# Kernel optimization log

Measured on AMD Instinct MI355X. Metric: run time of the kernel, lower is better.

## Reference

```python
import jax, jax.numpy as jnp
import numpy as np

N_NODES = 100000


def gcn_conv(x, W, b, src, dst, n):
    # PyG GCNConv: linear transform, add self-loops, symmetric degree normalization,
    # scatter-add aggregation from src -> dst, then bias.
    h = x @ W  # [N, F_out]
    loop = jnp.arange(n, dtype=src.dtype)
    s = jnp.concatenate([src, loop])  # sources incl. self-loops
    d = jnp.concatenate([dst, loop])  # targets incl. self-loops
    deg = jax.ops.segment_sum(jnp.ones_like(d, dtype=h.dtype), d, num_segments=n)
    dinv = jnp.where(deg > 0, jax.lax.rsqrt(deg), 0.0)
    norm = dinv[s] * dinv[d]  # [E+N]
    msg = h[s] * norm[:, None]  # gather + scale
    out = jax.ops.segment_sum(msg, d, num_segments=n)  # scatter-add
    return out + b


def setup_inputs() -> dict:
    key = jax.random.key(0)
    k1, k2, k3, k4 = jax.random.split(key, 4)
    n, e = N_NODES, 1600000
    z = jax.random.normal(k1, (n, 64), dtype=jnp.float32)
    edge_index = jax.random.randint(k2, (2, e), 0, n, dtype=jnp.int64)
    # Glorot-ish init for weights, zero bias (PyG default bias init is zeros)
    W1 = jax.random.normal(k3, (64, 128), dtype=jnp.float32) * (1.0 / np.sqrt(64))
    b1 = jnp.zeros((128,), dtype=jnp.float32)
    W2 = jax.random.normal(k4, (128, 64), dtype=jnp.float32) * (1.0 / np.sqrt(128))
    b2 = jnp.zeros((64,), dtype=jnp.float32)
    return {"z": z, "edge_index": edge_index, "W1": W1, "b1": b1, "W2": W2, "b2": b2}


def reference(z, edge_index, W1, b1, W2, b2):
    n = z.shape[0]
    src, dst = edge_index[0], edge_index[1]
    h = gcn_conv(z, W1, b1, src, dst, n)
    h = jax.nn.relu(h)
    x_hat = gcn_conv(h, W2, b2, src, dst, n)
    return x_hat
```

## Files before the change

### kernel.cpp

```cpp
#include <hip/hip_runtime.h>
#include <hip/hip_bf16.h>


#define WAVE 64
#define BSHIFT 8
#define NPB 256
#define CAP 5120
#define CH 4096
#define NBMAX 512

typedef __attribute__((ext_vector_type(8))) short bf16x8;
typedef __attribute__((ext_vector_type(4))) float f32x4;

__device__ inline float bf16_to_f32(unsigned short h) {
    return __uint_as_float(((unsigned int)h) << 16);
}
__device__ inline unsigned short f32_to_bf16(float f) {
    unsigned int x = __float_as_uint(f);
    return (unsigned short)((x + 0x7FFFu + ((x >> 16) & 1u)) >> 16);
}

__device__ inline float gather_rows16(const unsigned short* __restrict__ hs,
                                      const int* __restrict__ csr,
                                      int beg, int end, int lane, int zrow,
                                      float acc)
{
    for (int e = beg; e < end; e += 16) {
        int s[16];
#pragma unroll
        for (int j = 0; j < 16; ++j) s[j] = csr[e + j];
#pragma unroll
        for (int j = 0; j < 16; ++j)
            s[j] = (e + j < end) ? s[j] : zrow;
        float v[16];
#pragma unroll
        for (int j = 0; j < 16; ++j)
            v[j] = bf16_to_f32(hs[(size_t)s[j] * 64 + lane]);
        float t0 = ((v[0] + v[1]) + (v[2] + v[3])) + ((v[4] + v[5]) + (v[6] + v[7]));
        float t1 = ((v[8] + v[9]) + (v[10] + v[11])) + ((v[12] + v[13]) + (v[14] + v[15]));
        acc += t0 + t1;
    }
    return acc;
}

__global__ void prep(const float* __restrict__ W1, const float* __restrict__ W2,
                     unsigned short* __restrict__ W1t, unsigned short* __restrict__ W2t,
                     int* __restrict__ bcursor, int NB,
                     unsigned short* __restrict__ zr, int N)
{
    int i = blockIdx.x * blockDim.x + threadIdx.x;
    if (i < NB) bcursor[i] = 0;
    if (i < 64) zr[(size_t)N * 64 + i] = 0;
    if (i < 128 * 64) {
        int n = i >> 6, k = i & 63;
        W1t[i] = f32_to_bf16(W1[k * 128 + n]);
    }
    if (i < 64 * 128) {
        int n = i >> 7, k = i & 127;
        W2t[i] = f32_to_bf16(W2[k * 64 + n]);
    }
}

__global__ __launch_bounds__(256) void bin_edges(
        const int* __restrict__ src, const int* __restrict__ dst,
        int* __restrict__ bcursor, int2* __restrict__ ebuf, int E, int NB)
{
    __shared__ int hist[NBMAX];
    __shared__ int cur[NBMAX];
    const int t  = threadIdx.x;
    const int e0 = blockIdx.x * CH;

    for (int b = t; b < NB; b += 256) hist[b] = 0;
    __syncthreads();

#pragma unroll
    for (int j = 0; j < CH / 256; ++j) {
        int e = e0 + j * 256 + t;
        if (e < E) atomicAdd(&hist[dst[e] >> BSHIFT], 1);
    }
    __syncthreads();

    for (int b = t; b < NB; b += 256) {
        int c = hist[b];
        cur[b] = (c > 0) ? atomicAdd(&bcursor[b], c) : 0;
    }
    __syncthreads();

#pragma unroll
    for (int j = 0; j < CH / 256; ++j) {
        int e = e0 + j * 256 + t;
        if (e < E) {
            int s = src[e], d = dst[e];
            int b = d >> BSHIFT;
            int pos = atomicAdd(&cur[b], 1);
            ebuf[(size_t)b * CAP + pos] = make_int2(s, d);
        }
    }
}

__global__ __launch_bounds__(256) void build_csr(
        const int2* __restrict__ ebuf, const int* __restrict__ bcursor,
        const float* __restrict__ z, float* __restrict__ dinv,
        int* __restrict__ rbeg, int* __restrict__ rend,
        int* __restrict__ csr, unsigned short* __restrict__ u, int N)
{
    __shared__ int   h[NPB];
    __shared__ int   tmp[NPB];
    __shared__ float sdv[NPB];
    const int t   = threadIdx.x;
    const int b   = blockIdx.x;
    const int n0  = b << BSHIFT;
    const int cnt = bcursor[b];
    const size_t base = (size_t)b * CAP;

    h[t] = 0;
    __syncthreads();

    for (int i = t; i < cnt; i += 256)
        atomicAdd(&h[ebuf[base + i].y - n0], 1);
    __syncthreads();

    int deg = h[t];
    tmp[t] = deg;
    __syncthreads();
    for (int off = 1; off < 256; off <<= 1) {
        int x = (t >= off) ? tmp[t - off] : 0;
        __syncthreads();
        tmp[t] += x;
        __syncthreads();
    }
    int st = tmp[t] - deg;

    int node = n0 + t;
    float di = rsqrtf((float)deg + 1.0f);
    sdv[t] = di;
    if (node < N) {
        dinv[node] = di;
        rbeg[node] = (int)base + st;
        rend[node] = (int)base + st + deg;
    }
    h[t] = st;
    __syncthreads();

    for (int i = t; i < cnt; i += 256) {
        int2 e = ebuf[base + i];
        int p = atomicAdd(&h[e.y - n0], 1);
        csr[base + p] = e.x;
    }

    const int nloc = (N - n0 < NPB) ? (N - n0) : NPB;
    for (int i = t; i < nloc * 16; i += 256) {
        int r = i >> 4, kq = i & 15;
        float d2 = sdv[r];
        float4 v = ((const float4*)(z + (size_t)(n0 + r) * 64))[kq];
        ushort4 o;
        o.x = f32_to_bf16(v.x * d2);
        o.y = f32_to_bf16(v.y * d2);
        o.z = f32_to_bf16(v.z * d2);
        o.w = f32_to_bf16(v.w * d2);
        ((ushort4*)(u + (size_t)(n0 + r) * 64))[kq] = o;
    }
}

template<bool POST>
__global__ __launch_bounds__(256) void aggregate64_bf16(
        const unsigned short* __restrict__ hs, const int* __restrict__ rbeg,
        const int* __restrict__ rend, const int* __restrict__ csr,
        const float* __restrict__ dinv, const float* __restrict__ b,
        void* __restrict__ out_, int N)
{
    int node = (int)((blockIdx.x * (size_t)blockDim.x + threadIdx.x) >> 6);
    int lane = threadIdx.x & 63;
    if (node >= N) return;
    node = __builtin_amdgcn_readfirstlane(node);

    const int beg = rbeg[node];
    const int end = rend[node];

    float acc = bf16_to_f32(hs[(size_t)node * 64 + lane]);
    acc = gather_rows16(hs, csr, beg, end, lane, N, acc);

    if (POST) {
        float o = dinv[node] * acc + b[lane];
        __builtin_nontemporal_store(o, &((float*)out_)[(size_t)node * 64 + lane]);
    } else {
        __builtin_nontemporal_store(f32_to_bf16(acc),
            &((unsigned short*)out_)[(size_t)node * 64 + lane]);
    }
}

#define TILE 32
#define W1T_ST 72
#define W2T_ST 136
#define A_ST   72
#define X1_ST  136

__global__ __launch_bounds__(256) void gemm12_mfma(
        const unsigned short* __restrict__ agg1,
        const unsigned short* __restrict__ W1t,
        const float* __restrict__ b1,
        const unsigned short* __restrict__ W2t,
        const float* __restrict__ dinv,
        unsigned short* __restrict__ hs2, int N)
{
    __shared__ unsigned short sW1[128 * W1T_ST];
    __shared__ unsigned short sW2[64 * W2T_ST];
    __shared__ unsigned short sA[TILE * A_ST];
    __shared__ unsigned short sX[TILE * X1_ST];
    __shared__ float sdv[TILE];

    const int tid  = threadIdx.x;
    const int row0 = blockIdx.x * TILE;
    const int lane = tid & 63;
    const int wv   = tid >> 6;
    const int l16  = lane & 15;
    const int quad = lane >> 4;

    for (int i = tid; i < 128 * 8; i += 256) {
        int r = i >> 3, c = i & 7;
        *(uint4*)&sW1[r * W1T_ST + c * 8] = *(const uint4*)&W1t[r * 64 + c * 8];
    }
    for (int i = tid; i < 64 * 16; i += 256) {
        int r = i >> 4, c = i & 15;
        *(uint4*)&sW2[r * W2T_ST + c * 8] = *(const uint4*)&W2t[r * 128 + c * 8];
    }
    for (int i = tid; i < TILE * 8; i += 256) {
        int r = i >> 3, c = i & 7;
        int gr = row0 + r;
        uint4 v = make_uint4(0u, 0u, 0u, 0u);
        if (gr < N) v = *(const uint4*)&agg1[(size_t)gr * 64 + c * 8];
        *(uint4*)&sA[r * A_ST + c * 8] = v;
    }
    if (tid < TILE) {
        int gr = row0 + tid;
        sdv[tid] = (gr < N) ? dinv[gr] : 0.0f;
    }
    __syncthreads();

    {
        const int mt  = wv & 1;
        const int ntb = (wv >> 1) * 4;
        f32x4 acc[4];
#pragma unroll
        for (int t = 0; t < 4; ++t) acc[t] = (f32x4)0.0f;

#pragma unroll
        for (int k0 = 0; k0 < 64; k0 += 32) {
            bf16x8 af = *(const bf16x8*)&sA[(mt * 16 + l16) * A_ST + k0 + quad * 8];
#pragma unroll
            for (int t = 0; t < 4; ++t) {
                bf16x8 bf = *(const bf16x8*)&sW1[((ntb + t) * 16 + l16) * W1T_ST + k0 + quad * 8];
                acc[t] = __builtin_amdgcn_mfma_f32_16x16x32_bf16(af, bf, acc[t], 0, 0, 0);
            }
        }

#pragma unroll
        for (int t = 0; t < 4; ++t) {
            int col = (ntb + t) * 16 + l16;
            float bb = b1[col];
#pragma unroll
            for (int r = 0; r < 4; ++r) {
                int lr = mt * 16 + quad * 4 + r;
                float o = fmaxf(acc[t][r] * sdv[lr] + bb, 0.0f);
                sX[lr * X1_ST + col] = f32_to_bf16(o);
            }
        }
    }
    __syncthreads();

    {
        const int mt  = wv & 1;
        const int ntb = (wv >> 1) * 2;
        f32x4 acc[2];
#pragma unroll
        for (int t = 0; t < 2; ++t) acc[t] = (f32x4)0.0f;

#pragma unroll
        for (int k0 = 0; k0 < 128; k0 += 32) {
            bf16x8 af = *(const bf16x8*)&sX[(mt * 16 + l16) * X1_ST + k0 + quad * 8];
#pragma unroll
            for (int t = 0; t < 2; ++t) {
                bf16x8 bf = *(const bf16x8*)&sW2[((ntb + t) * 16 + l16) * W2T_ST + k0 + quad * 8];
                acc[t] = __builtin_amdgcn_mfma_f32_16x16x32_bf16(af, bf, acc[t], 0, 0, 0);
            }
        }

#pragma unroll
        for (int t = 0; t < 2; ++t) {
            int col = (ntb + t) * 16 + l16;
#pragma unroll
            for (int r = 0; r < 4; ++r) {
                int lr = mt * 16 + quad * 4 + r;
                int gr = row0 + lr;
                if (gr < N)
                    hs2[(size_t)gr * 64 + col] = f32_to_bf16(acc[t][r] * sdv[lr]);
            }
        }
    }
}

static inline size_t align_up(size_t x, size_t a) { return (x + a - 1) / a * a; }

extern "C" void kernel_launch(void* const* d_in, const int* in_sizes, int n_in,
                              void* d_out, int out_size, void* d_ws, size_t ws_size,
                              hipStream_t stream) {
    const float* z    = (const float*)d_in[0];
    const int*   eidx = (const int*)d_in[1];
    const float* W1   = (const float*)d_in[2];
    const float* b1   = (const float*)d_in[3];
    const float* W2   = (const float*)d_in[4];
    const float* b2   = (const float*)d_in[5];
    float* out = (float*)d_out;

    const int N = in_sizes[0] / 64;
    const int E = in_sizes[1] / 2;
    const int* src = eidx;
    const int* dst = eidx + E;
    const int NB = (N + NPB - 1) >> BSHIFT;

    char* ws = (char*)d_ws;
    size_t off = 0;
    float* dinv    = (float*)(ws + off); off = align_up(off + (size_t)N * 4, 512);
    int*   rbeg    = (int*)  (ws + off); off = align_up(off + (size_t)N * 4, 512);
    int*   rend    = (int*)  (ws + off); off = align_up(off + (size_t)N * 4, 512);
    int*   bcursor = (int*)  (ws + off); off = align_up(off + (size_t)NBMAX * 4, 512);
    unsigned short* W1t = (unsigned short*)(ws + off); off = align_up(off + 8192 * 2, 512);
    unsigned short* W2t = (unsigned short*)(ws + off); off = align_up(off + 8192 * 2, 512);
    int*   csr     = (int*)  (ws + off); off = align_up(off + (size_t)NB * CAP * 4, 512);
    float* bufA    = (float*)(ws + off); off = align_up(off + (size_t)N * 64 * 4, 512);
    float* bufB    = (float*)(ws + off); off = align_up(off + (size_t)N * 64 * 4, 512);
    float* bufC    = (float*)(ws + off); off = align_up(off + (size_t)N * 128 * 4, 512);
    (void)ws_size;

    unsigned short* u    = (unsigned short*)bufA;
    unsigned short* agg1 = (unsigned short*)bufB;
    unsigned short* hs2  = (unsigned short*)bufA;
    int2*  ebuf    = (int2*)bufC;

    prep<<<32, 256, 0, stream>>>(W1, W2, W1t, W2t, bcursor, NB, u, N);

    bin_edges<<<(E + CH - 1) / CH, 256, 0, stream>>>(src, dst, bcursor, ebuf, E, NB);
    build_csr<<<NB, 256, 0, stream>>>(ebuf, bcursor, z, dinv, rbeg, rend, csr, u, N);

    aggregate64_bf16<false><<<(N + 3) / 4, 256, 0, stream>>>(u, rbeg, rend, csr, dinv, nullptr, agg1, N);

    gemm12_mfma<<<(N + TILE - 1) / TILE, 256, 0, stream>>>(agg1, W1t, b1, W2t, dinv, hs2, N);

    aggregate64_bf16<true><<<(N + 3) / 4, 256, 0, stream>>>(hs2, rbeg, rend, csr, dinv, b2, out, N);
}
```

Measured before the change: 236.9 us.

## Pack binned edges into 32-bit words and aggregate two nodes per wavefront

Edge binning now stores each edge as one 32-bit word: the source index sits in the low 24 bits and the destination's offset within its bin in the high 8 bits. This halves the ebuf write and read traffic between bin_edges and build_csr. The aggregation kernels now process two nodes per wavefront with interleaved gathers, putting more independent loads in flight. The packing assumes node ids fit in 24 bits, and the paired loop runs to the longer row, so it pads the shorter one with zero-row gathers.

```diff
diff --git a/kernel.cpp b/kernel.cpp
--- a/kernel.cpp
+++ b/kernel.cpp
@@ -20,29 +20,6 @@
     return (unsigned short)((x + 0x7FFFu + ((x >> 16) & 1u)) >> 16);
 }
 
-__device__ inline float gather_rows16(const unsigned short* __restrict__ hs,
-                                      const int* __restrict__ csr,
-                                      int beg, int end, int lane, int zrow,
-                                      float acc)
-{
-    for (int e = beg; e < end; e += 16) {
-        int s[16];
-#pragma unroll
-        for (int j = 0; j < 16; ++j) s[j] = csr[e + j];
-#pragma unroll
-        for (int j = 0; j < 16; ++j)
-            s[j] = (e + j < end) ? s[j] : zrow;
-        float v[16];
-#pragma unroll
-        for (int j = 0; j < 16; ++j)
-            v[j] = bf16_to_f32(hs[(size_t)s[j] * 64 + lane]);
-        float t0 = ((v[0] + v[1]) + (v[2] + v[3])) + ((v[4] + v[5]) + (v[6] + v[7]));
-        float t1 = ((v[8] + v[9]) + (v[10] + v[11])) + ((v[12] + v[13]) + (v[14] + v[15]));
-        acc += t0 + t1;
-    }
-    return acc;
-}
-
 __global__ void prep(const float* __restrict__ W1, const float* __restrict__ W2,
                      unsigned short* __restrict__ W1t, unsigned short* __restrict__ W2t,
                      int* __restrict__ bcursor, int NB,
@@ -63,7 +40,7 @@
 
 __global__ __launch_bounds__(256) void bin_edges(
         const int* __restrict__ src, const int* __restrict__ dst,
-        int* __restrict__ bcursor, int2* __restrict__ ebuf, int E, int NB)
+        int* __restrict__ bcursor, unsigned int* __restrict__ ebuf, int E, int NB)
 {
     __shared__ int hist[NBMAX];
     __shared__ int cur[NBMAX];
@@ -93,13 +70,14 @@
             int s = src[e], d = dst[e];
             int b = d >> BSHIFT;
             int pos = atomicAdd(&cur[b], 1);
-            ebuf[(size_t)b * CAP + pos] = make_int2(s, d);
+            ebuf[(size_t)b * CAP + pos] =
+                (unsigned int)s | ((unsigned int)(d & (NPB - 1)) << 24);
         }
     }
 }
 
 __global__ __launch_bounds__(256) void build_csr(
-        const int2* __restrict__ ebuf, const int* __restrict__ bcursor,
+        const unsigned int* __restrict__ ebuf, const int* __restrict__ bcursor,
         const float* __restrict__ z, float* __restrict__ dinv,
         int* __restrict__ rbeg, int* __restrict__ rend,
         int* __restrict__ csr, unsigned short* __restrict__ u, int N)
@@ -117,7 +95,7 @@
     __syncthreads();
 
     for (int i = t; i < cnt; i += 256)
-        atomicAdd(&h[ebuf[base + i].y - n0], 1);
+        atomicAdd(&h[ebuf[base + i] >> 24], 1);
     __syncthreads();
 
     int deg = h[t];
@@ -143,9 +121,9 @@
     __syncthreads();
 
     for (int i = t; i < cnt; i += 256) {
-        int2 e = ebuf[base + i];
-        int p = atomicAdd(&h[e.y - n0], 1);
-        csr[base + p] = e.x;
+        unsigned int w = ebuf[base + i];
+        int p = atomicAdd(&h[w >> 24], 1);
+        csr[base + p] = (int)(w & 0xFFFFFFu);
     }
 
     const int nloc = (N - n0 < NPB) ? (N - n0) : NPB;
@@ -169,23 +147,65 @@
         const float* __restrict__ dinv, const float* __restrict__ b,
         void* __restrict__ out_, int N)
 {
-    int node = (int)((blockIdx.x * (size_t)blockDim.x + threadIdx.x) >> 6);
-    int lane = threadIdx.x & 63;
-    if (node >= N) return;
-    node = __builtin_amdgcn_readfirstlane(node);
-
-    const int beg = rbeg[node];
-    const int end = rend[node];
-
-    float acc = bf16_to_f32(hs[(size_t)node * 64 + lane]);
-    acc = gather_rows16(hs, csr, beg, end, lane, N, acc);
+    int pair = (int)((blockIdx.x * (size_t)blockDim.x + threadIdx.x) >> 6);
+    const int lane = threadIdx.x & 63;
+    int nA = pair * 2;
+    if (nA >= N) return;
+    nA = __builtin_amdgcn_readfirstlane(nA);
+    const int nBr = nA + 1;
+    const bool hasB = (nBr < N);
+    const int nB = hasB ? nBr : N;
+
+    const int begA = rbeg[nA], endA = rend[nA];
+    int begB = 0, endB = 0;
+    if (hasB) { begB = rbeg[nBr]; endB = rend[nBr]; }
+
+    float accA = bf16_to_f32(hs[(size_t)nA * 64 + lane]);
+    float accB = bf16_to_f32(hs[(size_t)nB * 64 + lane]);
+
+    int nbat = (endA - begA + 15) >> 4;
+    int nbB  = (endB - begB + 15) >> 4;
+    if (nbB > nbat) nbat = nbB;
+
+    int eA = begA, eB = begB;
+    for (int bt = 0; bt < nbat; ++bt, eA += 16, eB += 16) {
+        int sA[16], sB[16];
+#pragma unroll
+        for (int j = 0; j < 16; ++j) sA[j] = csr[eA + j];
+#pragma unroll
+        for (int j = 0; j < 16; ++j) sB[j] = csr[eB + j];
+#pragma unroll
+        for (int j = 0; j < 16; ++j) sA[j] = (eA + j < endA) ? sA[j] : N;
+#pragma unroll
+        for (int j = 0; j < 16; ++j) sB[j] = (eB + j < endB) ? sB[j] : N;
+        float vA[16], vB[16];
+#pragma unroll
+        for (int j = 0; j < 16; ++j)
+            vA[j] = bf16_to_f32(hs[(size_t)sA[j] * 64 + lane]);
+#pragma unroll
+        for (int j = 0; j < 16; ++j)
+            vB[j] = bf16_to_f32(hs[(size_t)sB[j] * 64 + lane]);
+        float a0 = ((vA[0]+vA[1])+(vA[2]+vA[3])) + ((vA[4]+vA[5])+(vA[6]+vA[7]));
+        float a1 = ((vA[8]+vA[9])+(vA[10]+vA[11])) + ((vA[12]+vA[13])+(vA[14]+vA[15]));
+        accA += a0 + a1;
+        float c0 = ((vB[0]+vB[1])+(vB[2]+vB[3])) + ((vB[4]+vB[5])+(vB[6]+vB[7]));
+        float c1 = ((vB[8]+vB[9])+(vB[10]+vB[11])) + ((vB[12]+vB[13])+(vB[14]+vB[15]));
+        accB += c0 + c1;
+    }
 
     if (POST) {
-        float o = dinv[node] * acc + b[lane];
-        __builtin_nontemporal_store(o, &((float*)out_)[(size_t)node * 64 + lane]);
+        float oA = dinv[nA] * accA + b[lane];
+        __builtin_nontemporal_store(oA, &((float*)out_)[(size_t)nA * 64 + lane]);
+        if (hasB) {
+            float oB = dinv[nBr] * accB + b[lane];
+            __builtin_nontemporal_store(oB, &((float*)out_)[(size_t)nBr * 64 + lane]);
+        }
     } else {
-        __builtin_nontemporal_store(f32_to_bf16(acc),
-            &((unsigned short*)out_)[(size_t)node * 64 + lane]);
+        __builtin_nontemporal_store(f32_to_bf16(accA),
+            &((unsigned short*)out_)[(size_t)nA * 64 + lane]);
+        if (hasB)
+            __builtin_nontemporal_store(f32_to_bf16(accB),
+                &((unsigned short*)out_)[(size_t)nBr * 64 + lane]);
     }
 }
 
@@ -335,16 +355,24 @@
     unsigned short* u    = (unsigned short*)bufA;
     unsigned short* agg1 = (unsigned short*)bufB;
     unsigned short* hs2  = (unsigned short*)bufA;
-    int2*  ebuf    = (int2*)bufC;
+    unsigned int*   ebuf = (unsigned int*)bufC;
 
     prep<<<32, 256, 0, stream>>>(W1, W2, W1t, W2t, bcursor, NB, u, N);
 
     bin_edges<<<(E + CH - 1) / CH, 256, 0, stream>>>(src, dst, bcursor, ebuf, E, NB);
     build_csr<<<NB, 256, 0, stream>>>(ebuf, bcursor, z, dinv, rbeg, rend, csr, u, N);
 
-    aggregate64_bf16<false><<<(N + 3) / 4, 256, 0, stream>>>(u, rbeg, rend, csr, dinv, nullptr, agg1, N);
+    {
+        int pairs = (N + 1) / 2;
+        aggregate64_bf16<false><<<(pairs + 3) / 4, 256, 0, stream>>>(
+            u, rbeg, rend, csr, dinv, nullptr, agg1, N);
+    }
 
     gemm12_mfma<<<(N + TILE - 1) / TILE, 256, 0, stream>>>(agg1, W1t, b1, W2t, dinv, hs2, N);
 
-    aggregate64_bf16<true><<<(N + 3) / 4, 256, 0, stream>>>(hs2, rbeg, rend, csr, dinv, b2, out, N);
-}
+    {
+        int pairs = (N + 1) / 2;
+        aggregate64_bf16<true><<<(pairs + 3) / 4, 256, 0, stream>>>(
+            hs2, rbeg, rend, csr, dinv, b2, out, N);
+    }
+}
```

Measured after the change: 234.0 us. No clear change (-1.2%).
